# Optimization experiments

Hardware: AMD Instinct MI355X
Metric: run time of the kernel (lower is better)

Reference implementation:

```python
import jax, jax.numpy as jnp
import numpy as np

B, T, E, H, FF = 8, 1024, 1024, 16, 4096
HD = E // H
SCALE = HD ** -0.5
EPS = 1e-12  # LayerNorm eps from TransformerLayer


def layer_norm(x, w, b):
    u = x.mean(-1, keepdims=True)
    s = ((x - u) ** 2).mean(-1, keepdims=True)  # biased variance, as in module
    return w * (x - u) / jnp.sqrt(s + EPS) + b


def setup_inputs() -> dict:
    key = jax.random.key(0)
    ks = jax.random.split(key, 8)
    std = 0.02  # nn.init.normal_(std=0.02)
    x = jax.random.normal(ks[0], (B, T, E), jnp.float32)
    # padding mask: positions >= length are padding (1 = ignore); ensure no all-masked row
    lengths = jax.random.randint(ks[1], (B,), T // 2, T + 1)
    self_padding_mask = jnp.arange(T)[None, :] >= lengths[:, None]
    # causal mask from SelfAttentionMask: triu(ones, 1)
    attn_mask = jnp.triu(jnp.ones((T, T), dtype=bool), 1)
    in_w = std * jax.random.normal(ks[2], (3 * E, E), jnp.float32)
    in_b = jnp.zeros((3 * E,), jnp.float32)
    out_w = std * jax.random.normal(ks[3], (E, E), jnp.float32)
    out_b = jnp.zeros((E,), jnp.float32)
    fc1_w = std * jax.random.normal(ks[4], (FF, E), jnp.float32)
    fc1_b = jnp.zeros((FF,), jnp.float32)
    fc2_w = std * jax.random.normal(ks[5], (E, FF), jnp.float32)
    fc2_b = jnp.zeros((E,), jnp.float32)
    ln1_w = jnp.ones((E,), jnp.float32)
    ln1_b = jnp.zeros((E,), jnp.float32)
    ln2_w = jnp.ones((E,), jnp.float32)
    ln2_b = jnp.zeros((E,), jnp.float32)
    return dict(x=x, in_w=in_w, in_b=in_b, out_w=out_w, out_b=out_b,
                fc1_w=fc1_w, fc1_b=fc1_b, fc2_w=fc2_w, fc2_b=fc2_b,
                ln1_w=ln1_w, ln1_b=ln1_b, ln2_w=ln2_w, ln2_b=ln2_b,
                self_padding_mask=self_padding_mask, attn_mask=attn_mask)


def reference(x, in_w, in_b, out_w, out_b, fc1_w, fc1_b, fc2_w, fc2_b,
              ln1_w, ln1_b, ln2_w, ln2_b, self_padding_mask, attn_mask):
    b, t, e = x.shape
    # --- self attention sublayer ---
    residual = x
    qkv = x @ in_w.T + in_b                       # [B,T,3E] fused in_proj (qkv_same path)
    q, k, v = jnp.split(qkv, 3, axis=-1)
    q = (q * SCALE).reshape(b, t, H, HD)
    k = k.reshape(b, t, H, HD)
    v = v.reshape(b, t, H, HD)
    scores = jnp.einsum('bqhd,bkhd->bhqk', q, k)  # [B,H,T,T]
    mask = attn_mask[None, None, :, :] | self_padding_mask[:, None, None, :]
    scores = jnp.where(mask, -jnp.inf, scores)
    p = jax.nn.softmax(scores, axis=-1)
    attn = jnp.einsum('bhqk,bkhd->bqhd', p, v).reshape(b, t, e)
    attn = attn @ out_w.T + out_b
    x = layer_norm(residual + attn, ln1_w, ln1_b)
    # --- feed-forward sublayer ---
    residual = x
    h = jax.nn.relu(x @ fc1_w.T + fc1_b)
    x = layer_norm(residual + (h @ fc2_w.T + fc2_b), ln2_w, ln2_b)
    return x
```

## Files before the change

### kernel.cpp

```cpp
#include <hip/hip_runtime.h>

typedef unsigned short u16;
typedef __attribute__((ext_vector_type(8))) short short8;
typedef __attribute__((ext_vector_type(4))) short short4v;
typedef __attribute__((ext_vector_type(4))) float f32x4;

#define DEV static __device__ __forceinline__

DEV float bf2f(u16 h) {
    union { unsigned int u; float f; } v; v.u = ((unsigned int)h) << 16; return v.f;
}
DEV u16 f2bf(float f) {
    union { float f; unsigned int u; } v; v.f = f;
    unsigned int r = (v.u + 0x7fff + ((v.u >> 16) & 1)) >> 16;
    return (u16)r;
}
DEV float ldx(const void* p, size_t i, int f32) {
    return f32 ? ((const float*)p)[i] : bf2f(((const u16*)p)[i]);
}

#define QSCL 0.18033688011112042f

#define GLD16(g, l) __builtin_amdgcn_global_load_lds( \
    (const __attribute__((address_space(1))) void*)(g), \
    (__attribute__((address_space(3))) void*)(l), 16, 0, 0)

#define STAGE(P, pf32, eoff, dst8) do {                                        \
    if (!(pf32)) { GLD16(((const u16*)(P)) + (eoff), (dst8)); }                \
    else {                                                                     \
        const float* _p = ((const float*)(P)) + (eoff);                        \
        f32x4 _a = *(const f32x4*)_p, _b = *(const f32x4*)(_p + 4);            \
        short8 _s;                                                             \
        _s[0]=(short)f2bf(_a[0]); _s[1]=(short)f2bf(_a[1]);                    \
        _s[2]=(short)f2bf(_a[2]); _s[3]=(short)f2bf(_a[3]);                    \
        _s[4]=(short)f2bf(_b[0]); _s[5]=(short)f2bf(_b[1]);                    \
        _s[6]=(short)f2bf(_b[2]); _s[7]=(short)f2bf(_b[3]);                    \
        *(short8*)(dst8) = _s;                                                 \
    } } while (0)

__global__ __launch_bounds__(64) void probe_kernel(
    const void* __restrict__ x, const void* __restrict__ pad,
    int* __restrict__ flags, int* __restrict__ flagsA)
{
    const int lane = threadIdx.x;
    const u16* xu = (const u16*)x;
    const unsigned int e = (xu[lane * 2] >> 7) & 0xFF;
    const int sane = (e >= 0x70 && e <= 0x8F) ? 1 : 0;
    unsigned long long m = __ballot(sane);
    const int f32 = (__popcll(m) < 32) ? 1 : 0;

    const unsigned int* pi = (const unsigned int*)pad;
    int bytes = 0;
#pragma unroll
    for (int j = 0; j < 6; j++) {
        unsigned int v = pi[128 + j * 64 + lane];
        if (v > 1u) bytes = 1;
    }
    m = __ballot(bytes);
    if (lane == 0) {
        flags[0] = f32; flags[1] = (m != 0ULL) ? 1 : 0;
        flagsA[0] = 0;  flagsA[1] = 0;
    }
}

__global__ __launch_bounds__(256) void conv4(
    const void* __restrict__ src, u16* __restrict__ dst, int n4,
    const int* __restrict__ flags)
{
    const int i = blockIdx.x * 256 + threadIdx.x;
    if (i >= n4) return;
    if (flags[0]) {
        f32x4 v = ((const f32x4*)src)[i];
        short4v s;
        s[0] = (short)f2bf(v[0]); s[1] = (short)f2bf(v[1]);
        s[2] = (short)f2bf(v[2]); s[3] = (short)f2bf(v[3]);
        ((short4v*)dst)[i] = s;
    } else {
        ((short4v*)dst)[i] = ((const short4v*)src)[i];
    }
}

__global__ __launch_bounds__(256) void mask_to_bias(
    const void* __restrict__ pad, float* __restrict__ out,
    const int* __restrict__ flags)
{
    const int i = blockIdx.x * 256 + threadIdx.x;
    const int mv = flags[1] ? (int)((const unsigned char*)pad)[i]
                            : ((const int*)pad)[i];
    out[i] = mv ? -1e30f : 0.0f;
}

#define GEMM_CORE(Av, ASEL, a_row0, Wv, w_off, ldw, K)                        \
    __shared__ __align__(16) u16 As[128 * 32];                                \
    __shared__ __align__(16) u16 Bs[128 * 32];                                \
    const int inf32 = flags[0];                                               \
    const int af32  = (ASEL) ? inf32 : 0;                                     \
    const int tid  = threadIdx.x;                                             \
    const int lane = tid & 63;                                                \
    const int wave = tid >> 6;                                                \
    const int lc   = lane & 15;                                               \
    const int quad = lane >> 4;                                               \
    const int m0 = blockIdx.x * 128;                                          \
    const int n0 = blockIdx.y * 128;                                          \
    const int wm = (wave >> 1) * 64;                                          \
    const int wn = (wave & 1) * 64;                                           \
    const int r0 = tid >> 2;                                                  \
    const int ko = (tid & 3) * 8;                                             \
    f32x4 acc[4][4] = {};                                                     \
    for (int k0 = 0; k0 < (K); k0 += 32) {                                    \
        STAGE(Av, af32, ((size_t)(a_row0) + m0 + r0) * (K) + k0 + ko,         \
              &As[tid * 8]);                                                  \
        STAGE(Av, af32, ((size_t)(a_row0) + m0 + r0 + 64) * (K) + k0 + ko,    \
              &As[2048 + tid * 8]);                                           \
        STAGE(Wv, inf32, (size_t)(w_off) + (size_t)(n0 + r0) * (ldw) + k0 + ko,\
              &Bs[tid * 8]);                                                  \
        STAGE(Wv, inf32, (size_t)(w_off) + (size_t)(n0 + r0 + 64) * (ldw) + k0 + ko,\
              &Bs[2048 + tid * 8]);                                           \
        __syncthreads();                                                      \
        short8 afr[4], bfr[4];                                                \
        const int qd = quad * 8;                                              \
        _Pragma("unroll")                                                     \
        for (int mt = 0; mt < 4; mt++)                                        \
            afr[mt] = *(const short8*)&As[(wm + mt * 16 + lc) * 32 + qd];     \
        _Pragma("unroll")                                                     \
        for (int nt = 0; nt < 4; nt++)                                        \
            bfr[nt] = *(const short8*)&Bs[(wn + nt * 16 + lc) * 32 + qd];     \
        _Pragma("unroll")                                                     \
        for (int mt = 0; mt < 4; mt++)                                        \
            _Pragma("unroll")                                                 \
            for (int nt = 0; nt < 4; nt++)                                    \
                acc[mt][nt] = __builtin_amdgcn_mfma_f32_16x16x32_bf16(        \
                    afr[mt], bfr[nt], acc[mt][nt], 0, 0, 0);                  \
        __syncthreads();                                                      \
    }                                                                         \
    const int ce0 = n0 + wn + lc;                                             \
    const int re0 = m0 + wm + quad * 4;

template<int EPI>
__global__ __launch_bounds__(256, 2) void gemm_bt(
    const void* __restrict__ A, int a_sel, long a_row0,
    const void* __restrict__ W, long w_off,
    const void* __restrict__ bias, long b_off,
    const void* __restrict__ resid, int r_sel, long r_row0,
    u16* __restrict__ C, long c_row0,
    int N, int K, int ldw, const int* __restrict__ flags)
{
    GEMM_CORE(A, a_sel, a_row0, W, w_off, ldw, K)
    const int rf32 = r_sel ? inf32 : 0;
#pragma unroll
    for (int mt = 0; mt < 4; mt++) {
#pragma unroll
        for (int nt = 0; nt < 4; nt++) {
            const int c = ce0 + nt * 16;
            const float bv = ldx(bias, (size_t)b_off + c, inf32);
#pragma unroll
            for (int i = 0; i < 4; i++) {
                const int r = re0 + mt * 16 + i;
                float v = acc[mt][nt][i] + bv;
                if (EPI == 1)
                    v += ldx(resid, ((size_t)r_row0 + r) * N + c, rf32);
                if (EPI == 2) v = fmaxf(v, 0.0f);
                C[((size_t)c_row0 + r) * N + c] = f2bf(v);
            }
        }
    }
}

__global__ __launch_bounds__(256, 2) void gemm_qkv(
    const void* __restrict__ A, long a_row0,
    const void* __restrict__ W, const void* __restrict__ bias,
    u16* __restrict__ Qo, u16* __restrict__ Ko, u16* __restrict__ Vt,
    const int* __restrict__ flags)
{
    GEMM_CORE(A, 1, a_row0, W, 0, 1024, 1024)
    if (n0 < 1024) {
#pragma unroll
        for (int mt = 0; mt < 4; mt++)
#pragma unroll
            for (int nt = 0; nt < 4; nt++) {
                const int c = ce0 + nt * 16;
                const float bv = ldx(bias, c, inf32);
#pragma unroll
                for (int i = 0; i < 4; i++) {
                    const int r = re0 + mt * 16 + i;
                    Qo[((size_t)a_row0 + r) * 1024 + c] =
                        f2bf((acc[mt][nt][i] + bv) * QSCL);
                }
            }
    } else if (n0 < 2048) {
#pragma unroll
        for (int mt = 0; mt < 4; mt++)
#pragma unroll
            for (int nt = 0; nt < 4; nt++) {
                const int c = ce0 + nt * 16;
                const float bv = ldx(bias, c, inf32);
#pragma unroll
                for (int i = 0; i < 4; i++) {
                    const int r = re0 + mt * 16 + i;
                    Ko[(size_t)r * 1024 + (c - 1024)] = f2bf(acc[mt][nt][i] + bv);
                }
            }
    } else {
#pragma unroll
        for (int mt = 0; mt < 4; mt++)
#pragma unroll
            for (int nt = 0; nt < 4; nt++) {
                const int c = ce0 + nt * 16;
                const float bv = ldx(bias, c, inf32);
                const int cv = c - 2048;
                const int hh = cv >> 6, d = cv & 63;
                const int rb = re0 + mt * 16;
                const int bl = rb >> 10, t = rb & 1023;
                short4v pk;
#pragma unroll
                for (int i = 0; i < 4; i++)
                    pk[i] = (short)f2bf(acc[mt][nt][i] + bv);
                *(short4v*)&Vt[((size_t)(bl * 16 + hh) * 64 + d) * 1024 + t] = pk;
            }
    }
}

__global__ __launch_bounds__(256, 2) void gemm_accf32(
    const void* __restrict__ A, const void* __restrict__ W, long w_off,
    const void* __restrict__ bias, const u16* __restrict__ resid, long r_row0,
    float* __restrict__ C, int ldw, int init, const int* __restrict__ flags)
{
    GEMM_CORE(A, 0, 0, W, w_off, ldw, 1024)
#pragma unroll
    for (int mt = 0; mt < 4; mt++) {
#pragma unroll
        for (int nt = 0; nt < 4; nt++) {
            const int c = ce0 + nt * 16;
            const float bv = ldx(bias, c, inf32);
#pragma unroll
            for (int i = 0; i < 4; i++) {
                const int r = re0 + mt * 16 + i;
                float v = acc[mt][nt][i];
                if (init) v += bv + bf2f(resid[((size_t)r_row0 + r) * 1024 + c]);
                else      v += C[(size_t)r * 1024 + c];
                C[(size_t)r * 1024 + c] = v;
            }
        }
    }
}

#define GEMM8_PRE(Ag_, Wg_, Kg_)                                              \
    __shared__ __align__(16) u16 Ab[3][128 * 64];                             \
    __shared__ __align__(16) u16 Bb[3][256 * 64];                             \
    const u16* Ag = (Ag_); const u16* Wg = (Wg_); const int Kg = (Kg_);       \
    const int tid  = threadIdx.x;                                             \
    const int lane = tid & 63;                                                \
    const int lc   = lane & 15;                                               \
    const int quad = lane >> 4;                                               \
    const int w    = tid >> 6;                                                \
    const int wr   = w >> 2;                                                  \
    const int wc   = w & 3;                                                   \
    const int m0 = blockIdx.x * 128;                                          \
    const int n0 = blockIdx.y * 256;                                          \
    const int srow = tid >> 3;                                                \
    const int scol = (((tid & 7) ^ (srow & 7)) << 3);                         \
    const int sw0 = (((quad) ^ (lc & 7)) << 3);                               \
    const int sw1 = sw0 ^ 32;                                                 \
    f32x4 acc[4][4] = {};                                                     \
    short8 af[4], bf[4];

#define SA8(buf, kk) do {                                                     \
    GLD16(Ag + (size_t)(m0 + srow) * Kg + (kk) + scol, &Ab[buf][tid * 8]);    \
    GLD16(Ag + (size_t)(m0 + 64 + srow) * Kg + (kk) + scol,                   \
          &Ab[buf][4096 + tid * 8]); } while (0)
#define SB8a(buf, kk) do {                                                    \
    GLD16(Wg + (size_t)(n0 + srow) * Kg + (kk) + scol, &Bb[buf][tid * 8]);    \
    GLD16(Wg + (size_t)(n0 + 64 + srow) * Kg + (kk) + scol,                   \
          &Bb[buf][4096 + tid * 8]); } while (0)
#define SB8b(buf, kk) do {                                                    \
    GLD16(Wg + (size_t)(n0 + 128 + srow) * Kg + (kk) + scol,                  \
          &Bb[buf][8192 + tid * 8]);                                          \
    GLD16(Wg + (size_t)(n0 + 192 + srow) * Kg + (kk) + scol,                  \
          &Bb[buf][12288 + tid * 8]); } while (0)
#define LDFR(rbuf, SW) do { _Pragma("unroll")                                 \
    for (int q_ = 0; q_ < 4; q_++) {                                          \
        af[q_] = *(const short8*)&Ab[rbuf][(wr * 64 + q_ * 16 + lc) * 64 + (SW)];\
        bf[q_] = *(const short8*)&Bb[rbuf][(wc * 64 + q_ * 16 + lc) * 64 + (SW)];\
    } } while (0)
#define MFMA16 do { _Pragma("unroll")                                         \
    for (int mq = 0; mq < 4; mq++) { _Pragma("unroll")                        \
    for (int nq = 0; nq < 4; nq++)                                            \
        acc[mq][nq] = __builtin_amdgcn_mfma_f32_16x16x32_bf16(                \
            af[mq], bf[nq], acc[mq][nq], 0, 0, 0); } } while (0)

#define GEMM8_LOOP                                                            \
    const int NT = Kg >> 6;                                                   \
    SA8(0, 0); SB8a(0, 0); SB8b(0, 0);                                        \
    if (NT > 1) { SA8(1, 64); SB8a(1, 64); SB8b(1, 64); }                     \
    if (NT > 1) asm volatile("s_waitcnt vmcnt(6)" ::: "memory");              \
    else        asm volatile("s_waitcnt vmcnt(0)" ::: "memory");              \
    __builtin_amdgcn_s_barrier();                                             \
    int rb_ = 0, wb_ = 2;                                                     \
    for (int t = 0; t < NT; ++t) {                                            \
        const bool s_ = (t + 2 < NT);                                         \
        const int k2_ = (t + 2) << 6;                                         \
        LDFR(rb_, sw0);                                                       \
        if (s_) { SA8(wb_, k2_); SB8a(wb_, k2_); }                            \
        __builtin_amdgcn_s_barrier();                                         \
        asm volatile("s_waitcnt lgkmcnt(0)" ::: "memory");                    \
        __builtin_amdgcn_s_setprio(1);                                        \
        MFMA16;                                                               \
        __builtin_amdgcn_s_setprio(0);                                        \
        __builtin_amdgcn_s_barrier();                                         \
        LDFR(rb_, sw1);                                                       \
        if (s_) SB8b(wb_, k2_);                                               \
        __builtin_amdgcn_s_barrier();                                         \
        asm volatile("s_waitcnt lgkmcnt(0)" ::: "memory");                    \
        __builtin_amdgcn_s_setprio(1);                                        \
        MFMA16;                                                               \
        __builtin_amdgcn_s_setprio(0);                                        \
        if (s_) asm volatile("s_waitcnt vmcnt(6)" ::: "memory");              \
        else    asm volatile("s_waitcnt vmcnt(0)" ::: "memory");              \
        __builtin_amdgcn_s_barrier();                                         \
        rb_ = (rb_ == 2) ? 0 : rb_ + 1;                                      \
        wb_ = (wb_ == 2) ? 0 : wb_ + 1;                                      \
    }                                                                         \
    const int cb0 = n0 + wc * 64 + lc;                                        \
    const int rb0 = m0 + wr * 64 + quad * 4;

template<int EPI>
__global__ __launch_bounds__(512, 2) void gemm8(
    const u16* __restrict__ A, const u16* __restrict__ W,
    const u16* __restrict__ bias, const u16* __restrict__ resid,
    u16* __restrict__ C, int N, int K)
{
    GEMM8_PRE(A, W, K)
    GEMM8_LOOP
#pragma unroll
    for (int mq = 0; mq < 4; mq++) {
#pragma unroll
        for (int nq = 0; nq < 4; nq++) {
            const int cN = cb0 + nq * 16;
            const float bv = bf2f(bias[cN]);
#pragma unroll
            for (int i = 0; i < 4; i++) {
                const int rM = rb0 + mq * 16 + i;
                float v = acc[mq][nq][i] + bv;
                if (EPI == 1) v += bf2f(resid[(size_t)rM * N + cN]);
                if (EPI == 2) v = fmaxf(v, 0.0f);
                C[(size_t)rM * N + cN] = f2bf(v);
            }
        }
    }
}

#define GEMM256_PRE(Ag_, Wg_, Kg_)                                            \
    __shared__ __align__(16) u16 Ab[3][8192];                                 \
    __shared__ __align__(16) u16 Bb[3][8192];                                 \
    const u16* Ag = (Ag_); const u16* Wg = (Wg_); const int Kg = (Kg_);       \
    const int tid  = threadIdx.x;                                             \
    const int lane = tid & 63;                                                \
    const int lc   = lane & 15;                                               \
    const int quad = lane >> 4;                                               \
    const int w    = tid >> 6;                                                \
    const int wr   = w >> 2;                                                  \
    const int wc   = w & 3;                                                   \
    const int m0 = blockIdx.x * 256;                                          \
    const int n0 = blockIdx.y * 256;                                          \
    const int s_r = tid >> 2;                                                 \
    const int s_c = (((tid & 3) ^ ((tid >> 3) & 3)) << 3);                    \
    const int fsw = ((quad ^ ((lc >> 1) & 3)) << 3);                          \
    const int arow = wr * 128 + lc;                                           \
    const int brow = wc * 64 + lc;                                            \
    f32x4 acc[8][4] = {};                                                     \
    short8 af[4], bf[4];

#define SA256(buf, kk) do {                                                   \
    GLD16(Ag + (size_t)(m0 + s_r) * Kg + (kk) + s_c, &Ab[buf][tid * 8]);      \
    GLD16(Ag + (size_t)(m0 + 128 + s_r) * Kg + (kk) + s_c,                    \
          &Ab[buf][4096 + tid * 8]); } while (0)
#define SB256(buf, kk) do {                                                   \
    GLD16(Wg + (size_t)(n0 + s_r) * Kg + (kk) + s_c, &Bb[buf][tid * 8]);      \
    GLD16(Wg + (size_t)(n0 + 128 + s_r) * Kg + (kk) + s_c,                    \
          &Bb[buf][4096 + tid * 8]); } while (0)
#define LDA256(MH) do { _Pragma("unroll")                                     \
    for (int q_ = 0; q_ < 4; q_++)                                            \
        af[q_] = *(const short8*)                                             \
            &Ab[rb_][(arow + ((MH) * 4 + q_) * 16) * 32 + fsw]; } while (0)
#define LDB256 do { _Pragma("unroll")                                         \
    for (int q_ = 0; q_ < 4; q_++)                                            \
        bf[q_] = *(const short8*)                                             \
            &Bb[rb_][(brow + q_ * 16) * 32 + fsw]; } while (0)
#define MF256(MH) do { _Pragma("unroll")                                      \
    for (int mq = 0; mq < 4; mq++) { _Pragma("unroll")                        \
    for (int nq = 0; nq < 4; nq++)                                            \
        acc[(MH) * 4 + mq][nq] = __builtin_amdgcn_mfma_f32_16x16x32_bf16(     \
            af[mq], bf[nq], acc[(MH) * 4 + mq][nq], 0, 0, 0); } } while (0)

#define GEMM256_LOOP                                                          \
    const int NT = Kg >> 5;                                                   \
    SA256(0, 0); SB256(0, 0);                                                 \
    if (NT > 1) { SA256(1, 32); SB256(1, 32); }                               \
    if (NT > 1) asm volatile("s_waitcnt vmcnt(4)" ::: "memory");              \
    else        asm volatile("s_waitcnt vmcnt(0)" ::: "memory");              \
    __builtin_amdgcn_s_barrier();                                             \
    int rb_ = 0, wb_ = 2;                                                     \
    for (int t = 0; t < NT; ++t) {                                            \
        const bool s_ = (t + 2 < NT);                                         \
        const int k2_ = (t + 2) << 5;                                         \
        LDB256; LDA256(0);                                                    \
        if (s_) SA256(wb_, k2_);                                              \
        __builtin_amdgcn_s_barrier();                                         \
        asm volatile("s_waitcnt lgkmcnt(0)" ::: "memory");                    \
        __builtin_amdgcn_s_setprio(1);                                        \
        MF256(0);                                                             \
        __builtin_amdgcn_s_setprio(0);                                        \
        __builtin_amdgcn_s_barrier();                                         \
        LDA256(1);                                                            \
        if (s_) SB256(wb_, k2_);                                              \
        __builtin_amdgcn_s_barrier();                                         \
        asm volatile("s_waitcnt lgkmcnt(0)" ::: "memory");                    \
        __builtin_amdgcn_s_setprio(1);                                        \
        MF256(1);                                                             \
        __builtin_amdgcn_s_setprio(0);                                        \
        if (s_) asm volatile("s_waitcnt vmcnt(4)" ::: "memory");              \
        else    asm volatile("s_waitcnt vmcnt(0)" ::: "memory");              \
        __builtin_amdgcn_s_barrier();                                         \
        rb_ = (rb_ == 2) ? 0 : rb_ + 1;                                      \
        wb_ = (wb_ == 2) ? 0 : wb_ + 1;                                      \
    }                                                                         \
    const int cb0 = n0 + wc * 64 + lc;                                        \
    const int rb0 = m0 + wr * 128 + quad * 4;

template<int EPI>
__global__ __launch_bounds__(512, 2) void gemm256(
    const u16* __restrict__ A, const u16* __restrict__ W,
    const u16* __restrict__ bias, const u16* __restrict__ resid,
    u16* __restrict__ C, int N, int K)
{
    GEMM256_PRE(A, W, K)
    GEMM256_LOOP
#pragma unroll
    for (int mq = 0; mq < 8; mq++) {
#pragma unroll
        for (int nq = 0; nq < 4; nq++) {
            const int cN = cb0 + nq * 16;
            const float bv = bf2f(bias[cN]);
#pragma unroll
            for (int i = 0; i < 4; i++) {
                const int rM = rb0 + mq * 16 + i;
                float v = acc[mq][nq][i] + bv;
                if (EPI == 1) v += bf2f(resid[(size_t)rM * N + cN]);
                if (EPI == 2) v = fmaxf(v, 0.0f);
                C[(size_t)rM * N + cN] = f2bf(v);
            }
        }
    }
}

__global__ __launch_bounds__(512, 2) void gemm256_qkv(
    const u16* __restrict__ A, const u16* __restrict__ W,
    const u16* __restrict__ bias,
    u16* __restrict__ Qo, u16* __restrict__ Ko, u16* __restrict__ Vt)
{
    GEMM256_PRE(A, W, 1024)
    GEMM256_LOOP
    if (n0 < 1024) {
#pragma unroll
        for (int mq = 0; mq < 8; mq++)
#pragma unroll
            for (int nq = 0; nq < 4; nq++) {
                const int c = cb0 + nq * 16;
                const float bv = bf2f(bias[c]);
#pragma unroll
                for (int i = 0; i < 4; i++) {
                    const int r = rb0 + mq * 16 + i;
                    Qo[(size_t)r * 1024 + c] =
                        f2bf((acc[mq][nq][i] + bv) * QSCL);
                }
            }
    } else if (n0 < 2048) {
#pragma unroll
        for (int mq = 0; mq < 8; mq++)
#pragma unroll
            for (int nq = 0; nq < 4; nq++) {
                const int c = cb0 + nq * 16;
                const float bv = bf2f(bias[c]);
#pragma unroll
                for (int i = 0; i < 4; i++) {
                    const int r = rb0 + mq * 16 + i;
                    Ko[(size_t)r * 1024 + (c - 1024)] =
                        f2bf(acc[mq][nq][i] + bv);
                }
            }
    } else {
#pragma unroll
        for (int mq = 0; mq < 8; mq++)
#pragma unroll
            for (int nq = 0; nq < 4; nq++) {
                const int c = cb0 + nq * 16;
                const float bv = bf2f(bias[c]);
                const int cv = c - 2048;
                const int hh = cv >> 6, d = cv & 63;
                const int rbase = rb0 + mq * 16;
                const int bl = rbase >> 10, tt = rbase & 1023;
                short4v pk;
#pragma unroll
                for (int i = 0; i < 4; i++)
                    pk[i] = (short)f2bf(acc[mq][nq][i] + bv);
                *(short4v*)&Vt[((size_t)(bl * 16 + hh) * 64 + d) * 1024 + tt] = pk;
            }
    }
}

__global__ __launch_bounds__(256, 2) void attn_kernel(
    u16* __restrict__ QO, const u16* __restrict__ Ko,
    const u16* __restrict__ Vt, const float* __restrict__ kb, int b0)
{
    __shared__ __align__(16) u16 Qs[2 * 128 * 32];
    __shared__ __align__(16) u16 Ks[2][2 * 64 * 32];
    __shared__ __align__(16) u16 Vs[2][2 * 64 * 32];
    __shared__ __align__(16) u16 Ps[4][32 * 72];
    __shared__ float kba[1024];

    const int tid  = threadIdx.x;
    const int lane = tid & 63;
    const int w    = tid >> 6;
    const int lc   = lane & 15;
    const int quad = lane >> 4;
    const int bl = blockIdx.y >> 4;
    const int h  = blockIdx.y & 15;
    const int b  = b0 + bl;

    short8 bsum;
    {
        const short ov = (lc == 0) ? (short)0x3F80 : (short)0;
#pragma unroll
        for (int j = 0; j < 8; j++) bsum[j] = ov;
    }

    *(f32x4*)&kba[tid * 4] = *(const f32x4*)&kb[b * 1024 + tid * 4];

    for (int p = 0; p < 2; p++) {
        const int qt = p ? 7 - (int)blockIdx.x : (int)blockIdx.x;

#pragma unroll
        for (int it = 0; it < 4; it++) {
            const int kcd = it >> 1, half = it & 1;
            const int r = half * 64 + (tid >> 2);
            const int c = kcd * 32 + (tid & 3) * 8;
            GLD16(&QO[((size_t)(b * 1024 + qt * 128 + r)) * 1024 + h * 64 + c],
                  &Qs[kcd * 4096 + half * 2048 + tid * 8]);
        }
        {
            const int rr = tid >> 2;
#pragma unroll
            for (int it = 0; it < 2; it++) {
                const int cc = it * 32 + (tid & 3) * 8;
                GLD16(&Ko[((size_t)(bl * 1024 + rr)) * 1024 + h * 64 + cc],
                      &Ks[0][it * 2048 + tid * 8]);
                GLD16(&Vt[((size_t)(bl * 16 + h) * 64 + rr) * 1024 + cc],
                      &Vs[0][it * 2048 + tid * 8]);
            }
        }
        __syncthreads();

        short8 aq[2][2];
#pragma unroll
        for (int mt = 0; mt < 2; mt++)
#pragma unroll
            for (int kc = 0; kc < 2; kc++)
                aq[mt][kc] = *(const short8*)
                    &Qs[kc * 4096 + (w * 32 + mt * 16 + lc) * 32 + quad * 8];

        f32x4 o[2][4] = {};
        float m_i[2][4], l_i[2][4];
#pragma unroll
        for (int mt = 0; mt < 2; mt++)
#pragma unroll
            for (int i = 0; i < 4; i++) { m_i[mt][i] = -1e30f; l_i[mt][i] = 0.0f; }

        const int ktmax = 2 * qt + 2;
        for (int kt = 0; kt < ktmax; kt++) {
            const int cur = kt & 1;
            if (kt + 1 < ktmax) {
                const int nxt = cur ^ 1;
                const int rr = tid >> 2;
#pragma unroll
                for (int it = 0; it < 2; it++) {
                    const int cc = it * 32 + (tid & 3) * 8;
                    GLD16(&Ko[((size_t)(bl * 1024 + (kt + 1) * 64 + rr)) * 1024 + h * 64 + cc],
                          &Ks[nxt][it * 2048 + tid * 8]);
                    GLD16(&Vt[((size_t)(bl * 16 + h) * 64 + rr) * 1024 + (kt + 1) * 64 + cc],
                          &Vs[nxt][it * 2048 + tid * 8]);
                }
            }

            short8 bk[4][2];
#pragma unroll
            for (int nt = 0; nt < 4; nt++)
#pragma unroll
                for (int kc = 0; kc < 2; kc++)
                    bk[nt][kc] = *(const short8*)
                        &Ks[cur][kc * 2048 + (nt * 16 + lc) * 32 + quad * 8];

            f32x4 s[2][4];
#pragma unroll
            for (int mt = 0; mt < 2; mt++)
#pragma unroll
                for (int nt = 0; nt < 4; nt++) {
                    f32x4 z = {};
#pragma unroll
                    for (int kc = 0; kc < 2; kc++)
                        z = __builtin_amdgcn_mfma_f32_16x16x32_bf16(
                            aq[mt][kc], bk[nt][kc], z, 0, 0, 0);
                    s[mt][nt] = z;
                }

#pragma unroll
            for (int mt = 0; mt < 2; mt++)
#pragma unroll
                for (int nt = 0; nt < 4; nt++) {
                    const float kbv = kba[kt * 64 + nt * 16 + lc];
#pragma unroll
                    for (int i = 0; i < 4; i++) s[mt][nt][i] += kbv;
                }
            if (kt >= 2 * qt) {
#pragma unroll
                for (int mt = 0; mt < 2; mt++) {
                    const int qg0 = qt * 128 + w * 32 + mt * 16 + quad * 4;
#pragma unroll
                    for (int nt = 0; nt < 4; nt++) {
                        const int kg = kt * 64 + nt * 16 + lc;
#pragma unroll
                        for (int i = 0; i < 4; i++)
                            if (kg > qg0 + i) s[mt][nt][i] = -1e30f;
                    }
                }
            }

            float al[2][4];
#pragma unroll
            for (int mt = 0; mt < 2; mt++) {
                float mnew[4];
#pragma unroll
                for (int i = 0; i < 4; i++) {
                    float rm = fmaxf(fmaxf(s[mt][0][i], s[mt][1][i]),
                                     fmaxf(s[mt][2][i], s[mt][3][i]));
                    rm = fmaxf(rm, __shfl_xor(rm, 1));
                    rm = fmaxf(rm, __shfl_xor(rm, 2));
                    rm = fmaxf(rm, __shfl_xor(rm, 4));
                    rm = fmaxf(rm, __shfl_xor(rm, 8));
                    const float mn = fmaxf(m_i[mt][i], rm);
                    al[mt][i] = exp2f(m_i[mt][i] - mn);
                    m_i[mt][i] = mn;
                    mnew[i] = mn;
                }
#pragma unroll
                for (int nt = 0; nt < 4; nt++)
#pragma unroll
                    for (int i = 0; i < 4; i++)
                        s[mt][nt][i] = exp2f(s[mt][nt][i] - mnew[i]);
#pragma unroll
                for (int nt = 0; nt < 4; nt++) {
#pragma unroll
                    for (int i2 = 0; i2 < 2; i2++) {
                        unsigned int pk;
                        asm("v_cvt_pk_bf16_f32 %0, %1, %2"
                            : "=v"(pk)
                            : "v"(s[mt][nt][2 * i2]), "v"(s[mt][nt][2 * i2 + 1]));
                        Ps[w][(mt * 16 + quad * 4 + 2 * i2) * 72 + nt * 16 + lc] =
                            (u16)pk;
                        Ps[w][(mt * 16 + quad * 4 + 2 * i2 + 1) * 72 + nt * 16 + lc] =
                            (u16)(pk >> 16);
                    }
                }
            }
            int chg = 0;
#pragma unroll
            for (int mt = 0; mt < 2; mt++)
#pragma unroll
                for (int i = 0; i < 4; i++)
                    chg |= (al[mt][i] != 1.0f) ? 1 : 0;
            const int dor = __any(chg);

            short8 ap[2][2], bv2[4][2];
#pragma unroll
            for (int mt = 0; mt < 2; mt++)
#pragma unroll
                for (int kc = 0; kc < 2; kc++)
                    ap[mt][kc] = *(const short8*)
                        &Ps[w][(mt * 16 + lc) * 72 + kc * 32 + quad * 8];
#pragma unroll
            for (int nt = 0; nt < 4; nt++)
#pragma unroll
                for (int kc = 0; kc < 2; kc++)
                    bv2[nt][kc] = *(const short8*)
                        &Vs[cur][kc * 2048 + (nt * 16 + lc) * 32 + quad * 8];

            f32x4 ls[2] = {};
#pragma unroll
            for (int mt = 0; mt < 2; mt++)
#pragma unroll
                for (int kc = 0; kc < 2; kc++)
                    ls[mt] = __builtin_amdgcn_mfma_f32_16x16x32_bf16(
                        ap[mt][kc], bsum, ls[mt], 0, 0, 0);

#pragma unroll
            for (int mt = 0; mt < 2; mt++)
#pragma unroll
                for (int nt = 0; nt < 4; nt++) {
                    f32x4 oo = o[mt][nt];
                    if (dor) {
#pragma unroll
                        for (int i = 0; i < 4; i++) oo[i] *= al[mt][i];
                    }
#pragma unroll
                    for (int kc = 0; kc < 2; kc++)
                        oo = __builtin_amdgcn_mfma_f32_16x16x32_bf16(
                            ap[mt][kc], bv2[nt][kc], oo, 0, 0, 0);
                    o[mt][nt] = oo;
                }
#pragma unroll
            for (int mt = 0; mt < 2; mt++)
#pragma unroll
                for (int i = 0; i < 4; i++)
                    l_i[mt][i] = l_i[mt][i] * al[mt][i] + ls[mt][i];

            __syncthreads();
        }

#pragma unroll
        for (int mt = 0; mt < 2; mt++)
#pragma unroll
            for (int i = 0; i < 4; i++) {
                const float lv = __shfl(l_i[mt][i], (lane & 48));
                const float inv = lv > 0.0f ? 1.0f / lv : 0.0f;
#pragma unroll
                for (int nt = 0; nt < 4; nt++) {
                    const int r = qt * 128 + w * 32 + mt * 16 + quad * 4 + i;
                    const int d = nt * 16 + lc;
                    QO[((size_t)(b * 1024 + r)) * 1024 + h * 64 + d] =
                        f2bf(o[mt][nt][i] * inv);
                }
            }
    }
}

template<int IN16, int OUTSEL>
__global__ __launch_bounds__(256) void ln_kernel(
    const void* __restrict__ yv, const void* __restrict__ w,
    const void* __restrict__ bb, void* __restrict__ o, long o_row0,
    const int* __restrict__ flags)
{
    const int row = blockIdx.x;
    const int tid = threadIdx.x;
    const int inf32 = flags[0];
    float x0, x1, x2, x3;
    if (IN16) {
        const u16* p = (const u16*)yv + (size_t)row * 1024 + tid * 4;
        short4v v = *(const short4v*)p;
        x0 = bf2f((u16)v[0]); x1 = bf2f((u16)v[1]);
        x2 = bf2f((u16)v[2]); x3 = bf2f((u16)v[3]);
    } else {
        const float* p = (const float*)yv + (size_t)row * 1024 + tid * 4;
        f32x4 v = *(const f32x4*)p;
        x0 = v[0]; x1 = v[1]; x2 = v[2]; x3 = v[3];
    }
    float s = x0 + x1 + x2 + x3;
    float q = x0 * x0 + x1 * x1 + x2 * x2 + x3 * x3;
#pragma unroll
    for (int off = 32; off; off >>= 1) {
        s += __shfl_xor(s, off);
        q += __shfl_xor(q, off);
    }
    __shared__ float sm[8];
    const int lane = tid & 63, wv = tid >> 6;
    if (lane == 0) { sm[wv] = s; sm[4 + wv] = q; }
    __syncthreads();
    const float ts = sm[0] + sm[1] + sm[2] + sm[3];
    const float tq = sm[4] + sm[5] + sm[6] + sm[7];
    const float mean = ts * (1.0f / 1024.0f);
    float var = tq * (1.0f / 1024.0f) - mean * mean;
    if (var < 0.0f) var = 0.0f;
    const float rinv = rsqrtf(var + 1e-12f);

    const size_t obase = ((size_t)o_row0 + row) * 1024 + tid * 4;
#pragma unroll
    for (int j = 0; j < 4; j++) {
        const int c = tid * 4 + j;
        float xv = (j == 0) ? x0 : (j == 1) ? x1 : (j == 2) ? x2 : x3;
        float v = ldx(w, c, inf32) * ((xv - mean) * rinv) + ldx(bb, c, inf32);
        if (OUTSEL && inf32) ((float*)o)[obase + j] = v;
        else                 ((u16*)o)[obase + j] = f2bf(v);
    }
}

extern "C" void kernel_launch(void* const* d_in, const int* in_sizes, int n_in,
                              void* d_out, int out_size, void* d_ws, size_t ws_size,
                              hipStream_t stream)
{
    const void* x     = d_in[0];
    const void* in_w  = d_in[1];
    const void* in_b  = d_in[2];
    const void* out_w = d_in[3];
    const void* out_b = d_in[4];
    const void* fc1_w = d_in[5];
    const void* fc1_b = d_in[6];
    const void* fc2_w = d_in[7];
    const void* fc2_b = d_in[8];
    const void* ln1w  = d_in[9];
    const void* ln1b  = d_in[10];
    const void* ln2w  = d_in[11];
    const void* ln2b  = d_in[12];
    const void* pad   = d_in[13];
    u16* outp = (u16*)d_out;
    char* ws = (char*)d_ws;
    dim3 blk(256);
    dim3 blk8(512);

    const size_t MB = 1024 * 1024;
    const bool bigWS = ws_size >= (105 * MB + 64 * 1024);

    if (bigWS) {
        u16*   xb   = (u16*)(ws + 0);
        u16*   x1   = (u16*)(ws + 0);
        u16*   w1b  = (u16*)(ws + 16 * MB);
        u16*   wob  = (u16*)(ws + 22 * MB);
        u16*   f1b  = (u16*)(ws + 24 * MB);
        u16*   f2b  = (u16*)(ws + 32 * MB);
        u16*   inbb = (u16*)(ws + 40 * MB);
        u16*   outbb= (u16*)(ws + 40 * MB + 8192);
        u16*   f1bb = (u16*)(ws + 40 * MB + 16384);
        u16*   f2bb = (u16*)(ws + 40 * MB + 24576);
        u16*   Ko   = (u16*)(ws + 41 * MB);
        u16*   Vt   = (u16*)(ws + 57 * MB);
        u16*   y1   = (u16*)(ws + 73 * MB);
        u16*   h    = (u16*)(ws + 41 * MB);
        u16*   y2   = (u16*)(ws + 16 * MB);
        int*   flags  = (int*)(ws + 105 * MB);
        int*   flagsA = (int*)(ws + 105 * MB + 32);
        float* kbias  = (float*)(ws + 105 * MB + 64);

        probe_kernel<<<dim3(1), dim3(64), 0, stream>>>(x, pad, flags, flagsA);
        mask_to_bias<<<dim3(32), blk, 0, stream>>>(pad, kbias, flags);
        conv4<<<dim3(8192), blk, 0, stream>>>(x, xb, 2097152, flags);
        conv4<<<dim3(3072), blk, 0, stream>>>(in_w, w1b, 786432, flags);
        conv4<<<dim3(1024), blk, 0, stream>>>(out_w, wob, 262144, flags);
        conv4<<<dim3(4096), blk, 0, stream>>>(fc1_w, f1b, 1048576, flags);
        conv4<<<dim3(4096), blk, 0, stream>>>(fc2_w, f2b, 1048576, flags);
        conv4<<<dim3(3), blk, 0, stream>>>(in_b, inbb, 768, flags);
        conv4<<<dim3(1), blk, 0, stream>>>(out_b, outbb, 256, flags);
        conv4<<<dim3(4), blk, 0, stream>>>(fc1_b, f1bb, 1024, flags);
        conv4<<<dim3(1), blk, 0, stream>>>(fc2_b, f2bb, 256, flags);

        gemm256_qkv<<<dim3(32, 12), blk8, 0, stream>>>(
            xb, w1b, inbb, outp, Ko, Vt);
        attn_kernel<<<dim3(4, 128), blk, 0, stream>>>(outp, Ko, Vt, kbias, 0);
        gemm8<1><<<dim3(64, 4), blk8, 0, stream>>>(
            outp, wob, outbb, xb, y1, 1024, 1024);
        ln_kernel<1, 0><<<dim3(8192), blk, 0, stream>>>(y1, ln1w, ln1b, x1, 0, flags);
        gemm256<2><<<dim3(32, 16), blk8, 0, stream>>>(
            x1, f1b, f1bb, nullptr, h, 4096, 1024);
        gemm8<1><<<dim3(64, 4), blk8, 0, stream>>>(
            h, f2b, f2bb, x1, y2, 1024, 4096);
        ln_kernel<1, 1><<<dim3(8192), blk, 0, stream>>>(y2, ln2w, ln2b, d_out, 0, flags);
    } else {
        u16*   Ko    = (u16*)(ws + 0);
        u16*   Vt    = (u16*)(ws + 4 * MB);
        u16*   y1h   = (u16*)(ws + 0);
        float* acc   = (float*)(ws + 0);
        u16*   hc    = (u16*)(ws + 8 * MB);
        int*   flags  = (int*)(ws + 12 * MB);
        int*   flagsA = (int*)(ws + 12 * MB + 32);
        float* kbias  = (float*)(ws + 12 * MB + 64);

        probe_kernel<<<dim3(1), dim3(64), 0, stream>>>(x, pad, flags, flagsA);
        mask_to_bias<<<dim3(32), blk, 0, stream>>>(pad, kbias, flags);

        for (int q = 0; q < 4; q++) {
            const long r0 = (long)q * 2048;
            gemm_qkv<<<dim3(16, 24), blk, 0, stream>>>(
                x, r0, in_w, in_b, outp, Ko, Vt, flags);
            attn_kernel<<<dim3(4, 32), blk, 0, stream>>>(
                outp, Ko, Vt, kbias, q * 2);
        }
        for (int hf = 0; hf < 2; hf++) {
            const long r0 = (long)hf * 4096;
            gemm_bt<1><<<dim3(32, 8), blk, 0, stream>>>(
                outp, 0, r0, out_w, 0, out_b, 0, x, 1, r0,
                y1h, 0, 1024, 1024, 1024, flags);
            ln_kernel<1, 0><<<dim3(4096), blk, 0, stream>>>(
                y1h, ln1w, ln1b, outp, r0, flags);
        }
        for (int q = 3; q >= 0; q--) {
            const long r0 = (long)q * 2048;
            for (int c = 0; c < 4; c++) {
                gemm_bt<2><<<dim3(16, 8), blk, 0, stream>>>(
                    outp, 0, r0, fc1_w, (long)c * 1024 * 1024, fc1_b, (long)c * 1024,
                    nullptr, 0, 0, hc, 0, 1024, 1024, 1024, flags);
                gemm_accf32<<<dim3(16, 8), blk, 0, stream>>>(
                    hc, fc2_w, (long)c * 1024, fc2_b, outp, r0,
                    acc, 4096, c == 0, flags);
            }
            ln_kernel<0, 1><<<dim3(2048), blk, 0, stream>>>(
                acc, ln2w, ln2b, d_out, r0, flags);
        }
    }
}
```

Baseline: 517.4 us.

## Restructure 256x256 GEMM pipeline into double-buffered 64-wide K steps

Replaces the triple-buffered 32-wide K staging with a double buffer holding two 32-wide halves per 64-wide K step. Global-to-LDS loads for the next step are issued in four quarter chunks interleaved with the MFMA phases, and the vmcnt waits are adjusted to match. The LDS XOR swizzle pattern also changes for both the store and read sides. LDS footprint grows from six to eight 16KB buffers, which may affect occupancy at two blocks per CU, and the hand-tuned waitcnt counts risk ordering errors.

```diff
diff --git a/kernel.cpp b/kernel.cpp
--- a/kernel.cpp
+++ b/kernel.cpp
@@ -350,8 +350,8 @@
 }
 
 #define GEMM256_PRE(Ag_, Wg_, Kg_)                                            \
-    __shared__ __align__(16) u16 Ab[3][8192];                                 \
-    __shared__ __align__(16) u16 Bb[3][8192];                                 \
+    __shared__ __align__(16) u16 Ab[2][2][8192];                              \
+    __shared__ __align__(16) u16 Bb[2][2][8192];                              \
     const u16* Ag = (Ag_); const u16* Wg = (Wg_); const int Kg = (Kg_);       \
     const int tid  = threadIdx.x;                                             \
     const int lane = tid & 63;                                                \
@@ -363,29 +363,31 @@
     const int m0 = blockIdx.x * 256;                                          \
     const int n0 = blockIdx.y * 256;                                          \
     const int s_r = tid >> 2;                                                 \
-    const int s_c = (((tid & 3) ^ ((tid >> 3) & 3)) << 3);                    \
-    const int fsw = ((quad ^ ((lc >> 1) & 3)) << 3);                          \
+    const int s_c = (((tid & 3) ^ ((tid >> 4) & 3)) << 3);                    \
+    const int fsw = ((quad ^ ((lc >> 2) & 3)) << 3);                          \
     const int arow = wr * 128 + lc;                                           \
     const int brow = wc * 64 + lc;                                            \
     f32x4 acc[8][4] = {};                                                     \
     short8 af[4], bf[4];
 
-#define SA256(buf, kk) do {                                                   \
-    GLD16(Ag + (size_t)(m0 + s_r) * Kg + (kk) + s_c, &Ab[buf][tid * 8]);      \
-    GLD16(Ag + (size_t)(m0 + 128 + s_r) * Kg + (kk) + s_c,                    \
-          &Ab[buf][4096 + tid * 8]); } while (0)
-#define SB256(buf, kk) do {                                                   \
-    GLD16(Wg + (size_t)(n0 + s_r) * Kg + (kk) + s_c, &Bb[buf][tid * 8]);      \
-    GLD16(Wg + (size_t)(n0 + 128 + s_r) * Kg + (kk) + s_c,                    \
-          &Bb[buf][4096 + tid * 8]); } while (0)
-#define LDA256(MH) do { _Pragma("unroll")                                     \
+#define SAH(buf, kk, tt) do {                                                 \
+    GLD16(Ag + (size_t)(m0 + s_r) * Kg + (tt) * 64 + (kk) * 32 + s_c,         \
+          &Ab[buf][kk][tid * 8]);                                             \
+    GLD16(Ag + (size_t)(m0 + 128 + s_r) * Kg + (tt) * 64 + (kk) * 32 + s_c,   \
+          &Ab[buf][kk][4096 + tid * 8]); } while (0)
+#define SBH(buf, kk, tt) do {                                                 \
+    GLD16(Wg + (size_t)(n0 + s_r) * Kg + (tt) * 64 + (kk) * 32 + s_c,         \
+          &Bb[buf][kk][tid * 8]);                                             \
+    GLD16(Wg + (size_t)(n0 + 128 + s_r) * Kg + (tt) * 64 + (kk) * 32 + s_c,   \
+          &Bb[buf][kk][4096 + tid * 8]); } while (0)
+#define LDA2(buf, kk, MH) do { _Pragma("unroll")                              \
     for (int q_ = 0; q_ < 4; q_++)                                            \
         af[q_] = *(const short8*)                                             \
-            &Ab[rb_][(arow + ((MH) * 4 + q_) * 16) * 32 + fsw]; } while (0)
-#define LDB256 do { _Pragma("unroll")                                         \
+            &Ab[buf][kk][(arow + ((MH) * 4 + q_) * 16) * 32 + fsw]; } while (0)
+#define LDB2(buf, kk) do { _Pragma("unroll")                                  \
     for (int q_ = 0; q_ < 4; q_++)                                            \
         bf[q_] = *(const short8*)                                             \
-            &Bb[rb_][(brow + q_ * 16) * 32 + fsw]; } while (0)
+            &Bb[buf][kk][(brow + q_ * 16) * 32 + fsw]; } while (0)
 #define MF256(MH) do { _Pragma("unroll")                                      \
     for (int mq = 0; mq < 4; mq++) { _Pragma("unroll")                        \
     for (int nq = 0; nq < 4; nq++)                                            \
@@ -393,36 +395,56 @@
             af[mq], bf[nq], acc[(MH) * 4 + mq][nq], 0, 0, 0); } } while (0)
 
 #define GEMM256_LOOP                                                          \
-    const int NT = Kg >> 5;                                                   \
-    SA256(0, 0); SB256(0, 0);                                                 \
-    if (NT > 1) { SA256(1, 32); SB256(1, 32); }                               \
-    if (NT > 1) asm volatile("s_waitcnt vmcnt(4)" ::: "memory");              \
+    const int NT = Kg >> 6;                                                   \
+    SAH(0, 0, 0); SBH(0, 0, 0); SAH(0, 1, 0); SBH(0, 1, 0);                   \
+    if (NT > 1) SAH(1, 0, 1);                                                 \
+    if (NT > 1) asm volatile("s_waitcnt vmcnt(2)" ::: "memory");              \
     else        asm volatile("s_waitcnt vmcnt(0)" ::: "memory");              \
     __builtin_amdgcn_s_barrier();                                             \
-    int rb_ = 0, wb_ = 2;                                                     \
     for (int t = 0; t < NT; ++t) {                                            \
-        const bool s_ = (t + 2 < NT);                                         \
-        const int k2_ = (t + 2) << 5;                                         \
-        LDB256; LDA256(0);                                                    \
-        if (s_) SA256(wb_, k2_);                                              \
+        const int c_ = t & 1, nx_ = c_ ^ 1;                                   \
+        const bool s1_ = (t + 1 < NT), s2_ = (t + 2 < NT);                    \
+                                                          \
+        LDB2(c_, 0); LDA2(c_, 0, 0);                                          \
+        if (s1_) SBH(nx_, 0, t + 1);                                          \
         __builtin_amdgcn_s_barrier();                                         \
         asm volatile("s_waitcnt lgkmcnt(0)" ::: "memory");                    \
         __builtin_amdgcn_s_setprio(1);                                        \
         MF256(0);                                                             \
         __builtin_amdgcn_s_setprio(0);                                        \
         __builtin_amdgcn_s_barrier();                                         \
-        LDA256(1);                                                            \
-        if (s_) SB256(wb_, k2_);                                              \
+                                         \
+        LDA2(c_, 0, 1);                                                       \
+        if (s1_) SAH(nx_, 1, t + 1);                                          \
         __builtin_amdgcn_s_barrier();                                         \
         asm volatile("s_waitcnt lgkmcnt(0)" ::: "memory");                    \
         __builtin_amdgcn_s_setprio(1);                                        \
         MF256(1);                                                             \
         __builtin_amdgcn_s_setprio(0);                                        \
-        if (s_) asm volatile("s_waitcnt vmcnt(4)" ::: "memory");              \
-        else    asm volatile("s_waitcnt vmcnt(0)" ::: "memory");              \
-        __builtin_amdgcn_s_barrier();                                         \
-        rb_ = (rb_ == 2) ? 0 : rb_ + 1;                                      \
-        wb_ = (wb_ == 2) ? 0 : wb_ + 1;                                      \
+        if (s1_) asm volatile("s_waitcnt vmcnt(6)" ::: "memory");             \
+        else     asm volatile("s_waitcnt vmcnt(0)" ::: "memory");             \
+        __builtin_amdgcn_s_barrier();                                         \
+                                                          \
+        LDB2(c_, 1); LDA2(c_, 1, 0);                                          \
+        if (s1_) SBH(nx_, 1, t + 1);                                          \
+        __builtin_amdgcn_s_barrier();                                         \
+        asm volatile("s_waitcnt lgkmcnt(0)" ::: "memory");                    \
+        __builtin_amdgcn_s_setprio(1);                                        \
+        MF256(0);                                                             \
+        __builtin_amdgcn_s_setprio(0);                                        \
+        __builtin_amdgcn_s_barrier();                                         \
+                \
+        LDA2(c_, 1, 1);                                                       \
+        if (s2_) SAH(c_, 0, t + 2);                                           \
+        __builtin_amdgcn_s_barrier();                                         \
+        asm volatile("s_waitcnt lgkmcnt(0)" ::: "memory");                    \
+        __builtin_amdgcn_s_setprio(1);                                        \
+        MF256(1);                                                             \
+        __builtin_amdgcn_s_setprio(0);                                        \
+        if (s2_)      asm volatile("s_waitcnt vmcnt(6)" ::: "memory");        \
+        else if (s1_) asm volatile("s_waitcnt vmcnt(4)" ::: "memory");        \
+        else          asm volatile("s_waitcnt vmcnt(0)" ::: "memory");        \
+        __builtin_amdgcn_s_barrier();                                         \
     }                                                                         \
     const int cb0 = n0 + wc * 64 + lc;                                        \
     const int rb0 = m0 + wr * 128 + quad * 4;
```

Result: no change. 523.1 us (+1.1%).
